# Performance work log

Hardware: AMD Instinct MI355X
Metric: run time of the kernel (lower is better)

Reference implementation:

```python
import jax, jax.numpy as jnp
import numpy as np

B, N, DIM, H, HD = 8, 1024, 512, 8, 64
INNER = H * HD  # 512
KS = 5


def setup_inputs() -> dict:
    key = jax.random.key(0)
    ks = jax.random.split(key, 9)
    r = lambda k, shape, s=1.0: jax.random.normal(k, shape, dtype=jnp.float32) * s
    return {
        "x_1": r(ks[0], (B, N, DIM)),
        "x_2": r(ks[1], (B, N, DIM)),
        "Wqkv1": r(ks[2], (DIM, 4 * INNER), 0.02),
        "Wqkv2": r(ks[3], (DIM, 4 * INNER), 0.02),
        "Wout1": r(ks[4], (INNER, DIM), 0.02),
        "bout1": jnp.zeros((DIM,), jnp.float32),
        "Wout2": r(ks[5], (INNER, DIM), 0.02),
        "bout2": jnp.zeros((DIM,), jnp.float32),
        "conv_w": r(ks[6], (N, 1, KS), 0.1),   # depthwise Conv1d weight [out=N, in/groups=1, k]
        "conv_b": r(ks[7], (N,), 0.02),
    }


def _split_heads(t):
    # 'b n (h d) -> b h n d'
    b, n, _ = t.shape
    return t.reshape(b, n, H, HD).transpose(0, 2, 1, 3)


def _merge_heads(t):
    # 'b h n d -> b n (h d)'
    b, h, n, d = t.shape
    return t.transpose(0, 2, 1, 3).reshape(b, n, h * d)


def reference(x_1, x_2, Wqkv1, Wqkv2, Wout1, bout1, Wout2, bout2, conv_w, conv_b):
    scale = HD ** (-0.5)
    q1, k1, v1, s1 = map(_split_heads, jnp.split(x_1 @ Wqkv1, 4, axis=-1))
    q2, k2, v2, s2 = map(_split_heads, jnp.split(x_2 @ Wqkv2, 4, axis=-1))

    dots1 = jnp.einsum('bhid,bhjd->bhij', q1, k1) * scale
    dots2 = jnp.einsum('bhid,bhjd->bhij', q2, k2) * scale

    MS = _merge_heads(s1 + s2)  # [b, n, inner_dim]
    # depthwise conv over the feature axis, channels = tokens (n), kernel 5 pad 2
    A = jax.lax.conv_general_dilated(
        MS, conv_w, window_strides=(1,), padding=((KS // 2, KS // 2),),
        dimension_numbers=('NCH', 'OIH', 'NCH'), feature_group_count=N,
    ) + conv_b[None, :, None]
    MSg = jax.nn.sigmoid(A) * MS
    MSh = _split_heads(MSg)
    dots3 = jnp.einsum('bhid,bhjd->bhij', MSh, MSh) * scale

    a1 = jax.nn.softmax(dots1, axis=-1)
    a2 = jax.nn.softmax(dots2, axis=-1)
    a3 = jax.nn.softmax(dots3, axis=-1)

    t1 = jnp.einsum('bhij,bhjd->bhid', a3, v1) + v1
    t1 = jnp.einsum('bhij,bhjd->bhid', a1, t1)
    t2 = jnp.einsum('bhij,bhjd->bhid', a3, v2) + v2
    t2 = jnp.einsum('bhij,bhjd->bhid', a2, t2)

    out1 = _merge_heads(t1) @ Wout1 + bout1
    out2 = _merge_heads(t2) @ Wout2 + bout2
    return (out1, out2)
```

## Files before the change

kernel.cpp:

```cpp
#include <hip/hip_runtime.h>
#include <hip/hip_bf16.h>

#define B_     8
#define N_     1024
#define DIM_   512
#define H_     8
#define HD_    64
#define INNER_ 512
#define QKVC   2048
#define M_     8192

typedef __attribute__((ext_vector_type(8))) short short8;
typedef __attribute__((ext_vector_type(4))) float f32x4;
#define MFMA_BF16 __builtin_amdgcn_mfma_f32_16x16x32_bf16

__device__ __forceinline__ unsigned short f2b(float x) {
    __hip_bfloat16 h = __float2bfloat16(x);
    unsigned short u; __builtin_memcpy(&u, &h, 2); return u;
}
__device__ __forceinline__ unsigned int packsplit(float x) {
    unsigned int hb = f2b(x);
    float fh = __uint_as_float(hb << 16);
    unsigned int lb = f2b(x - fh);
    return (hb << 16) | lb;
}
__device__ __forceinline__ void split8(const float* v, short8& h, short8& l) {
#pragma unroll
    for (int i = 0; i < 8; i++) {
        unsigned int hb = f2b(v[i]);
        float fh = __uint_as_float(hb << 16);
        h[i] = (short)hb; l[i] = (short)f2b(v[i] - fh);
    }
}
__device__ __forceinline__ void split2x2(float a, float b, unsigned int& h, unsigned int& l) {
    unsigned int ha = f2b(a), hb = f2b(b);
    float fa = __uint_as_float(ha << 16), fb = __uint_as_float(hb << 16);
    h = ha | (hb << 16);
    l = (unsigned int)f2b(a - fa) | ((unsigned int)f2b(b - fb) << 16);
}

__device__ __forceinline__ void gll16(const unsigned short* g, unsigned short* l) {
    __builtin_amdgcn_global_load_lds(
        (const __attribute__((address_space(1))) void*)g,
        (__attribute__((address_space(3))) void*)l, 16, 0, 0);
}

__global__ __launch_bounds__(256)
void pack_a_tiled(const float* __restrict__ in, unsigned short* __restrict__ out)
{
    size_t i = ((size_t)blockIdx.x * 256 + threadIdx.x) * 4;
    float4 v = *(const float4*)(in + i);
    const size_t R = i >> 9;
    const int k  = (int)(i & 511);
    const int kt = k >> 5, kk = k & 31;
    const int r  = (int)(R & 127);
    const size_t rt = R >> 7;
    unsigned short* tile = out + (((rt << 4) + kt) << 13) + r * 64;
    unsigned int h01, l01, h23, l23;
    split2x2(v.x, v.y, h01, l01);
    split2x2(v.z, v.w, h23, l23);
    uint2 hv; hv.x = h01; hv.y = h23;
    uint2 lv; lv.x = l01; lv.y = l23;
    const int s7 = r & 7;
    *(uint2*)&tile[(((kk >> 3)     ^ s7) << 3) + (kk & 7)] = hv;
    *(uint2*)&tile[((((kk >> 3)+4) ^ s7) << 3) + (kk & 7)] = lv;
}

__global__ __launch_bounds__(256)
void pack_w_tiled(const float* __restrict__ W, unsigned short* __restrict__ out, int N)
{
    const int n  = blockIdx.x * 256 + threadIdx.x;
    const int k0 = blockIdx.y * 4;
    float f0 = W[(size_t)(k0 + 0) * N + n];
    float f1 = W[(size_t)(k0 + 1) * N + n];
    float f2 = W[(size_t)(k0 + 2) * N + n];
    float f3 = W[(size_t)(k0 + 3) * N + n];
    const int r  = n & 127;
    const size_t rt = n >> 7;
    const int kt = k0 >> 5, kk = k0 & 31;
    unsigned short* tile = out + (((rt << 4) + kt) << 13) + r * 64;
    unsigned int h01, l01, h23, l23;
    split2x2(f0, f1, h01, l01);
    split2x2(f2, f3, h23, l23);
    uint2 hv; hv.x = h01; hv.y = h23;
    uint2 lv; lv.x = l01; lv.y = l23;
    const int s7 = r & 7;
    *(uint2*)&tile[(((kk >> 3)     ^ s7) << 3) + (kk & 7)] = hv;
    *(uint2*)&tile[((((kk >> 3)+4) ^ s7) << 3) + (kk & 7)] = lv;
}

__global__ __launch_bounds__(256)
void pack_wt(const float* __restrict__ W, unsigned int* __restrict__ Wt, int N)
{
    const int n = blockIdx.x * 256 + threadIdx.x;
    const int k0 = blockIdx.y * 4;
    uint4 p;
    p.x = packsplit(W[(size_t)(k0 + 0) * N + n]);
    p.y = packsplit(W[(size_t)(k0 + 1) * N + n]);
    p.z = packsplit(W[(size_t)(k0 + 2) * N + n]);
    p.w = packsplit(W[(size_t)(k0 + 3) * N + n]);
    *(uint4*)&Wt[(size_t)n * 512 + k0] = p;
}

template<bool BIAS, bool PACKK>
__global__ __launch_bounds__(256)
void gemm_gll(const unsigned short* __restrict__ At, const unsigned short* __restrict__ Bt,
              const float* __restrict__ bias, float* __restrict__ Cp,
              int M, int N)
{
    __shared__ __align__(16) unsigned short sA[128 * 64];
    __shared__ __align__(16) unsigned short sB[128 * 64];

    const int t    = threadIdx.x;
    const int lane = t & 63;
    const int w    = t >> 6;
    const int n16  = lane & 15, quad = lane >> 4;
    const int wm   = w >> 1, wn = w & 1;
    const int m0 = blockIdx.y * 128, n0 = blockIdx.x * 128;

    f32x4 acc[4][4];
#pragma unroll
    for (int mt = 0; mt < 4; mt++)
#pragma unroll
        for (int nt = 0; nt < 4; nt++) acc[mt][nt] = (f32x4){0.f, 0.f, 0.f, 0.f};

    const unsigned short* Ag = At + ((size_t)blockIdx.y << 4) * 8192 + (w * 64 + lane) * 8;
    const unsigned short* Bg = Bt + ((size_t)blockIdx.x << 4) * 8192 + (w * 64 + lane) * 8;
    unsigned short* sAw = &sA[w * 512];
    unsigned short* sBw = &sB[w * 512];

    for (int kt = 0; kt < 16; kt++) {
        __syncthreads();
        const size_t ko = (size_t)kt * 8192;
#pragma unroll
        for (int i = 0; i < 4; i++) {
            gll16(Ag + ko + i * 2048, sAw + i * 2048);
            gll16(Bg + ko + i * 2048, sBw + i * 2048);
        }
        __syncthreads();

        short8 Ah[4], Al[4];
#pragma unroll
        for (int mt = 0; mt < 4; mt++) {
            const int row = 64 * wm + 16 * mt + n16;
            const int base = row * 64;
            const int s7 = row & 7;
            Ah[mt] = *(const short8*)&sA[base + (((quad    ) ^ s7) << 3)];
            Al[mt] = *(const short8*)&sA[base + (((quad + 4) ^ s7) << 3)];
        }
#pragma unroll
        for (int nt = 0; nt < 4; nt++) {
            const int row = 64 * wn + 16 * nt + n16;
            const int base = row * 64;
            const int s7 = row & 7;
            short8 Bh = *(const short8*)&sB[base + (((quad    ) ^ s7) << 3)];
            short8 Bl = *(const short8*)&sB[base + (((quad + 4) ^ s7) << 3)];
#pragma unroll
            for (int mt = 0; mt < 4; mt++) {
                acc[mt][nt] = MFMA_BF16(Ah[mt], Bh, acc[mt][nt], 0, 0, 0);
                acc[mt][nt] = MFMA_BF16(Al[mt], Bh, acc[mt][nt], 0, 0, 0);
                acc[mt][nt] = MFMA_BF16(Ah[mt], Bl, acc[mt][nt], 0, 0, 0);
            }
        }
    }

    const bool packout = PACKK && ((n0 >> 9) == 1);
    float bv[4];
#pragma unroll
    for (int nt = 0; nt < 4; nt++)
        bv[nt] = BIAS ? bias[n0 + 64 * wn + 16 * nt + n16] : 0.f;
#pragma unroll
    for (int mt = 0; mt < 4; mt++) {
        const int rbase = m0 + 64 * wm + 16 * mt + 4 * quad;
#pragma unroll
        for (int r = 0; r < 4; r++) {
#pragma unroll
            for (int nt = 0; nt < 4; nt++) {
                const int col = n0 + 64 * wn + 16 * nt + n16;
                const size_t off = (size_t)(rbase + r) * N + col;
                const float v = acc[mt][nt][r] + bv[nt];
                if (packout) ((unsigned int*)Cp)[off] = packsplit(v);
                else         Cp[off] = v;
            }
        }
    }
}

template<bool BIAS, bool PACKK>
__global__ __launch_bounds__(256)
void gemm_mfma(const unsigned int* __restrict__ Ap, const unsigned int* __restrict__ Btp,
               const float* __restrict__ bias, float* __restrict__ Cp,
               int M, int N)
{
    const int K = 512;
    __shared__ __align__(16) unsigned short sA[128 * 64];
    __shared__ __align__(16) unsigned short sB[128 * 64];

    const int t    = threadIdx.x;
    const int lane = t & 63;
    const int w    = t >> 6;
    const int n16  = lane & 15, quad = lane >> 4;
    const int wm   = w >> 1, wn = w & 1;
    const int m0 = blockIdx.y * 128, n0 = blockIdx.x * 128;

    f32x4 acc[4][4];
#pragma unroll
    for (int mt = 0; mt < 4; mt++)
#pragma unroll
        for (int nt = 0; nt < 4; nt++) acc[mt][nt] = (f32x4){0.f, 0.f, 0.f, 0.f};

    const int srow = t >> 1;
    const int kb   = (t & 1) * 16;
    const unsigned int* ag = Ap  + (size_t)(m0 + srow) * K + kb;
    const unsigned int* bg = Btp + (size_t)(n0 + srow) * K + kb;
    const int s7s = srow & 7;
    unsigned short* swA = &sA[srow * 64];
    unsigned short* swB = &sB[srow * 64];

    for (int k0 = 0; k0 < K; k0 += 32) {
        __syncthreads();
#pragma unroll
        for (int i = 0; i < 4; i++) {
            const int kk = kb + i * 4;
            const int ch = kk >> 3;
            const int ho = kk & 4;
            const int c_hi = ((ch    ) ^ s7s) << 3;
            const int c_lo = ((ch + 4) ^ s7s) << 3;
            uint4 va = *(const uint4*)(ag + k0 + i * 4);
            uint4 vb = *(const uint4*)(bg + k0 + i * 4);
            uint2 ha, la, hb, lb;
            ha.x = (va.y & 0xFFFF0000u) | (va.x >> 16);
            ha.y = (va.w & 0xFFFF0000u) | (va.z >> 16);
            la.x = (va.y << 16) | (va.x & 0xFFFFu);
            la.y = (va.w << 16) | (va.z & 0xFFFFu);
            hb.x = (vb.y & 0xFFFF0000u) | (vb.x >> 16);
            hb.y = (vb.w & 0xFFFF0000u) | (vb.z >> 16);
            lb.x = (vb.y << 16) | (vb.x & 0xFFFFu);
            lb.y = (vb.w << 16) | (vb.z & 0xFFFFu);
            *(uint2*)&swA[c_hi + ho] = ha;
            *(uint2*)&swA[c_lo + ho] = la;
            *(uint2*)&swB[c_hi + ho] = hb;
            *(uint2*)&swB[c_lo + ho] = lb;
        }
        __syncthreads();

        short8 Ah[4], Al[4];
#pragma unroll
        for (int mt = 0; mt < 4; mt++) {
            const int row = 64 * wm + 16 * mt + n16;
            const int base = row * 64;
            const int s7 = row & 7;
            Ah[mt] = *(const short8*)&sA[base + (((quad    ) ^ s7) << 3)];
            Al[mt] = *(const short8*)&sA[base + (((quad + 4) ^ s7) << 3)];
        }
#pragma unroll
        for (int nt = 0; nt < 4; nt++) {
            const int row = 64 * wn + 16 * nt + n16;
            const int base = row * 64;
            const int s7 = row & 7;
            short8 Bh = *(const short8*)&sB[base + (((quad    ) ^ s7) << 3)];
            short8 Bl = *(const short8*)&sB[base + (((quad + 4) ^ s7) << 3)];
#pragma unroll
            for (int mt = 0; mt < 4; mt++) {
                acc[mt][nt] = MFMA_BF16(Ah[mt], Bh, acc[mt][nt], 0, 0, 0);
                acc[mt][nt] = MFMA_BF16(Al[mt], Bh, acc[mt][nt], 0, 0, 0);
                acc[mt][nt] = MFMA_BF16(Ah[mt], Bl, acc[mt][nt], 0, 0, 0);
            }
        }
    }

    const bool packout = PACKK && ((n0 >> 9) == 1);
    float bv[4];
#pragma unroll
    for (int nt = 0; nt < 4; nt++)
        bv[nt] = BIAS ? bias[n0 + 64 * wn + 16 * nt + n16] : 0.f;
#pragma unroll
    for (int mt = 0; mt < 4; mt++) {
        const int rbase = m0 + 64 * wm + 16 * mt + 4 * quad;
#pragma unroll
        for (int r = 0; r < 4; r++) {
#pragma unroll
            for (int nt = 0; nt < 4; nt++) {
                const int col = n0 + 64 * wn + 16 * nt + n16;
                const size_t off = (size_t)(rbase + r) * N + col;
                const float v = acc[mt][nt][r] + bv[nt];
                if (packout) ((unsigned int*)Cp)[off] = packsplit(v);
                else         Cp[off] = v;
            }
        }
    }
}

__global__ __launch_bounds__(128)
void convgate_kernel(const float* __restrict__ qkv1, const float* __restrict__ qkv2,
                     const float* __restrict__ convw,
                     const float* __restrict__ convb,
                     float* __restrict__ MSg, unsigned int* __restrict__ MSgp)
{
    __shared__ float ms[INNER_];
    const int blk = blockIdx.x;
    const int n = blk & (N_ - 1);
    const int t = threadIdx.x;

    const float4* q1 = (const float4*)(qkv1 + (size_t)blk * QKVC + 3 * INNER_);
    const float4* q2 = (const float4*)(qkv2 + (size_t)blk * QKVC + 3 * INNER_);
    float4 v1 = q1[t], v2 = q2[t];
    float4 s;
    s.x = v1.x + v2.x; s.y = v1.y + v2.y; s.z = v1.z + v2.z; s.w = v1.w + v2.w;
    *(float4*)&ms[t * 4] = s;
    __syncthreads();

    float w[5];
#pragma unroll
    for (int k = 0; k < 5; k++) w[k] = convw[n * 5 + k];
    const float cb = convb[n];

    float out[4];
#pragma unroll
    for (int ff = 0; ff < 4; ff++) {
        int f = t * 4 + ff;
        float A = cb;
#pragma unroll
        for (int k = 0; k < 5; k++) {
            int idx = f + k - 2;
            if (idx >= 0 && idx < INNER_) A += ms[idx] * w[k];
        }
        float sg = 1.f / (1.f + __expf(-A));
        out[ff] = ms[f] * sg;
    }
    *(float4*)&MSg[(size_t)blk * INNER_ + t * 4] = make_float4(out[0], out[1], out[2], out[3]);
    uint4 p;
    p.x = packsplit(out[0]); p.y = packsplit(out[1]);
    p.z = packsplit(out[2]); p.w = packsplit(out[3]);
    *(uint4*)&MSgp[(size_t)blk * INNER_ + t * 4] = p;
}

template<int NV, bool RESID, bool PACKO, int NPROB>
__global__ __launch_bounds__(512, 2)
void mattn_kernel(const float* __restrict__ Q0, const float* __restrict__ Q1,
                  const unsigned int* __restrict__ K0, const unsigned int* __restrict__ K1,
                  const float* __restrict__ VA0, const float* __restrict__ VA1,
                  const float* __restrict__ VB0, const float* __restrict__ VB1,
                  float* __restrict__ OA0, float* __restrict__ OA1,
                  float* __restrict__ OB0, float* __restrict__ OB1,
                  long long q_sb, long long q_sh, int q_sr,
                  long long k_sb, long long k_sh, int k_sr,
                  long long v_sb, long long v_sh, int v_sr,
                  long long o_sb, long long o_sh, int o_sr)
{
    __shared__ __align__(16) unsigned short sK[64 * 128];
    __shared__ __align__(16) unsigned short sV0[64 * 64];
    __shared__ __align__(16) unsigned short sV1[(NV == 2) ? 64 * 64 : 8];
    __shared__ __align__(16) unsigned short sP[128 * 64];

    const int t    = threadIdx.x;
    const int w    = t >> 6;
    const int lane = t & 63;
    const int n16  = lane & 15;
    const int quad = lane >> 4;

    const int bid = blockIdx.x;
    const int c   = bid & 7;
    const int r1  = bid >> 3;
    const int qt  = r1 & 7;
    const int r2  = r1 >> 3;
    const int g   = r2 & 7;
    const int p   = (NPROB == 2) ? (r2 >> 3) : 0;
    const int bh  = 8 * g + c;
    const int b = bh >> 3, h = bh & 7;
    const int i0 = qt * 128;

    const float* Qb        = (NPROB == 2 && p) ? Q1 : Q0;
    const unsigned int* Kb = (NPROB == 2 && p) ? K1 : K0;
    const float* VAb       = (NPROB == 2 && p) ? VA1 : VA0;
    float* OAb             = (NPROB == 2 && p) ? OA1 : OA0;

    const float* Qg        = Qb  + (size_t)b * q_sb + (size_t)h * q_sh;
    const unsigned int* Kg = Kb  + (size_t)b * k_sb + (size_t)h * k_sh;
    const float* V0g       = VAb + (size_t)b * v_sb + (size_t)h * v_sh;
    const float* V1g = (NV == 2) ? (VB0 + (size_t)b * v_sb + (size_t)h * v_sh) : nullptr;
    float* O0g = OAb + (size_t)b * o_sb + (size_t)h * o_sh;
    float* O1g = (NV == 2) ? (OB0 + (size_t)b * o_sb + (size_t)h * o_sh) : nullptr;

    short8 Qh[2], Ql[2];
#pragma unroll
    for (int s = 0; s < 2; s++) {
        const float* qp = Qg + (size_t)(i0 + 16 * w + n16) * q_sr + 32 * s + 8 * quad;
        float qv[8];
        float4 q0 = *(const float4*)qp;
        float4 q1 = *(const float4*)(qp + 4);
        qv[0]=q0.x; qv[1]=q0.y; qv[2]=q0.z; qv[3]=q0.w;
        qv[4]=q1.x; qv[5]=q1.y; qv[6]=q1.z; qv[7]=q1.w;
        split8(qv, Qh[s], Ql[s]);
    }

    float m_ = -1e30f, l_ = 0.f;
    f32x4 O0a[4], O1a[(NV == 2) ? 4 : 1];
#pragma unroll
    for (int nt = 0; nt < 4; nt++) O0a[nt] = (f32x4){0.f,0.f,0.f,0.f};
    if constexpr (NV == 2) {
#pragma unroll
        for (int nt = 0; nt < 4; nt++) O1a[nt] = (f32x4){0.f,0.f,0.f,0.f};
    }

    const float scale = 0.125f;
    const int prow = 16 * w + n16;
    const int krow = t >> 3, kfc = t & 7;
    const int vc = t & 15, vp = t >> 4;

    for (int j0 = 0; j0 < N_; j0 += 64) {
        __syncthreads();

        {
            const unsigned int* kp = Kg + (size_t)(j0 + krow) * k_sr + 8 * kfc;
            uint4 va = *(const uint4*)kp;
            uint4 vb = *(const uint4*)(kp + 4);
            uint4 hi, lo;
            hi.x = (va.x >> 16) | (va.y & 0xFFFF0000u);
            hi.y = (va.z >> 16) | (va.w & 0xFFFF0000u);
            hi.z = (vb.x >> 16) | (vb.y & 0xFFFF0000u);
            hi.w = (vb.z >> 16) | (vb.w & 0xFFFF0000u);
            lo.x = (va.x & 0xFFFFu) | (va.y << 16);
            lo.y = (va.z & 0xFFFFu) | (va.w << 16);
            lo.z = (vb.x & 0xFFFFu) | (vb.y << 16);
            lo.w = (vb.z & 0xFFFFu) | (vb.w << 16);
            const int r15 = krow & 15;
            *(uint4*)&sK[krow * 128 + (((kfc    ) ^ r15) << 3)] = hi;
            *(uint4*)&sK[krow * 128 + (((kfc + 8) ^ r15) << 3)] = lo;
        }
        {
            const int j = 2 * vp;
            const float* a0 = V0g + (size_t)(j0 + j) * v_sr + 4 * vc;
            float4 va = *(const float4*)a0;
            float4 vb = *(const float4*)(a0 + v_sr);
#pragma unroll
            for (int e = 0; e < 4; e++) {
                float fa = (e==0)?va.x:(e==1)?va.y:(e==2)?va.z:va.w;
                float fb = (e==0)?vb.x:(e==1)?vb.y:(e==2)?vb.z:vb.w;
                unsigned int u = (unsigned int)f2b(fa) | ((unsigned int)f2b(fb) << 16);
                const int d = 4 * vc + e;
                const int phys = (vp >> 2) ^ ((d ^ (d >> 2)) & 7);
                *(unsigned int*)&sV0[d * 64 + (phys << 3) + (j & 7)] = u;
            }
            if constexpr (NV == 2) {
                const float* a1 = V1g + (size_t)(j0 + j) * v_sr + 4 * vc;
                float4 wa = *(const float4*)a1;
                float4 wb = *(const float4*)(a1 + v_sr);
#pragma unroll
                for (int e = 0; e < 4; e++) {
                    float fa = (e==0)?wa.x:(e==1)?wa.y:(e==2)?wa.z:wa.w;
                    float fb = (e==0)?wb.x:(e==1)?wb.y:(e==2)?wb.z:wb.w;
                    unsigned int u = (unsigned int)f2b(fa) | ((unsigned int)f2b(fb) << 16);
                    const int d = 4 * vc + e;
                    const int phys = (vp >> 2) ^ ((d ^ (d >> 2)) & 7);
                    *(unsigned int*)&sV1[d * 64 + (phys << 3) + (j & 7)] = u;
                }
            }
        }
        __syncthreads();

        f32x4 accS[4];
#pragma unroll
        for (int mt = 0; mt < 4; mt++) accS[mt] = (f32x4){0.f,0.f,0.f,0.f};
#pragma unroll
        for (int s = 0; s < 2; s++) {
#pragma unroll
            for (int mt = 0; mt < 4; mt++) {
                const unsigned short* kb2 = &sK[(16 * mt + n16) * 128];
                short8 kh = *(const short8*)&kb2[(((4*s + quad)    ) ^ n16) << 3];
                short8 kl = *(const short8*)&kb2[(((4*s + quad) + 8) ^ n16) << 3];
                accS[mt] = MFMA_BF16(kl, Qh[s], accS[mt], 0, 0, 0);
                accS[mt] = MFMA_BF16(kh, Ql[s], accS[mt], 0, 0, 0);
                accS[mt] = MFMA_BF16(kh, Qh[s], accS[mt], 0, 0, 0);
            }
        }

        float tmax = -1e30f;
#pragma unroll
        for (int mt = 0; mt < 4; mt++)
#pragma unroll
            for (int r = 0; r < 4; r++) tmax = fmaxf(tmax, accS[mt][r]);
        tmax *= scale;
        tmax = fmaxf(tmax, __shfl_xor(tmax, 16));
        tmax = fmaxf(tmax, __shfl_xor(tmax, 32));
        const float mnew = fmaxf(m_, tmax);
        const float alpha = __expf(m_ - mnew);
        m_ = mnew;
        float rsum = 0.f;
#pragma unroll
        for (int mt = 0; mt < 4; mt++) {
            float p0 = __expf(accS[mt][0] * scale - mnew);
            float p1 = __expf(accS[mt][1] * scale - mnew);
            float p2 = __expf(accS[mt][2] * scale - mnew);
            float p3 = __expf(accS[mt][3] * scale - mnew);
            rsum += (p0 + p1) + (p2 + p3);
            uint2 u;
            u.x = (unsigned int)f2b(p0) | ((unsigned int)f2b(p1) << 16);
            u.y = (unsigned int)f2b(p2) | ((unsigned int)f2b(p3) << 16);
            const int phys = (2 * mt + (quad >> 1)) ^ (n16 & 7);
            *(uint2*)&sP[prow * 64 + (phys << 3) + 4 * (quad & 1)] = u;
        }
        rsum += __shfl_xor(rsum, 16);
        rsum += __shfl_xor(rsum, 32);
        l_ = l_ * alpha + rsum;

        float ar[4];
#pragma unroll
        for (int r = 0; r < 4; r++) ar[r] = __shfl(alpha, (quad << 2) + r);
#pragma unroll
        for (int nt = 0; nt < 4; nt++) {
#pragma unroll
            for (int r = 0; r < 4; r++) O0a[nt][r] *= ar[r];
            if constexpr (NV == 2)
#pragma unroll
                for (int r = 0; r < 4; r++) O1a[nt][r] *= ar[r];
        }

#pragma unroll
        for (int s = 0; s < 2; s++) {
            short8 Pf = *(const short8*)&sP[prow * 64 + (((4*s + quad) ^ (n16 & 7)) << 3)];
#pragma unroll
            for (int nt = 0; nt < 4; nt++) {
                const int d = 16 * nt + n16;
                const int phys = (4*s + quad) ^ ((d ^ (d >> 2)) & 7);
                short8 vf = *(const short8*)&sV0[d * 64 + (phys << 3)];
                O0a[nt] = MFMA_BF16(Pf, vf, O0a[nt], 0, 0, 0);
                if constexpr (NV == 2) {
                    short8 vf1 = *(const short8*)&sV1[d * 64 + (phys << 3)];
                    O1a[nt] = MFMA_BF16(Pf, vf1, O1a[nt], 0, 0, 0);
                }
            }
        }
    }

    float linv[4];
#pragma unroll
    for (int r = 0; r < 4; r++) linv[r] = 1.0f / __shfl(l_, (quad << 2) + r);
#pragma unroll
    for (int r = 0; r < 4; r++) {
        const int row = i0 + 16 * w + 4 * quad + r;
#pragma unroll
        for (int nt = 0; nt < 4; nt++) {
            const int col = 16 * nt + n16;
            float v = O0a[nt][r] * linv[r];
            if constexpr (RESID) v += V0g[(size_t)row * v_sr + col];
            if constexpr (PACKO)
                ((unsigned int*)O0g)[(size_t)row * o_sr + col] = packsplit(v);
            else
                O0g[(size_t)row * o_sr + col] = v;
            if constexpr (NV == 2) {
                float v1 = O1a[nt][r] * linv[r];
                if constexpr (RESID) v1 += V1g[(size_t)row * v_sr + col];
                if constexpr (PACKO)
                    ((unsigned int*)O1g)[(size_t)row * o_sr + col] = packsplit(v1);
                else
                    O1g[(size_t)row * o_sr + col] = v1;
            }
        }
    }
}

extern "C" void kernel_launch(void* const* d_in, const int* in_sizes, int n_in,
                              void* d_out, int out_size, void* d_ws, size_t ws_size,
                              hipStream_t stream)
{
    const float* x1    = (const float*)d_in[0];
    const float* x2    = (const float*)d_in[1];
    const float* Wqkv1 = (const float*)d_in[2];
    const float* Wqkv2 = (const float*)d_in[3];
    const float* Wout1 = (const float*)d_in[4];
    const float* bout1 = (const float*)d_in[5];
    const float* Wout2 = (const float*)d_in[6];
    const float* bout2 = (const float*)d_in[7];
    const float* convw = (const float*)d_in[8];
    const float* convb = (const float*)d_in[9];

    const size_t QKV_ELEMS = (size_t)M_ * QKVC;
    const size_t BND_ELEMS = (size_t)M_ * INNER_;
    if (ws_size < (2 * QKV_ELEMS + 5 * BND_ELEMS) * sizeof(float)) return;

    float* ws   = (float*)d_ws;
    float* qkv1 = ws;
    float* qkv2 = qkv1 + QKV_ELEMS;
    float* MSg  = qkv2 + QKV_ELEMS;
    float* u1   = MSg + BND_ELEMS;
    float* u2   = u1 + BND_ELEMS;
    float* t1m  = u2 + BND_ELEMS;
    float* t2m  = t1m + BND_ELEMS;

    unsigned short* x1t = (unsigned short*)t1m;
    unsigned short* x2t = (unsigned short*)t2m;
    unsigned int*   MSgp = (unsigned int*)t1m;
    unsigned short* w1t = (unsigned short*)u2;
    unsigned short* w2t = w1t + (size_t)QKVC * DIM_ * 2;
    unsigned int*   wo1pt = (unsigned int*)u1;
    unsigned int*   wo2pt = wo1pt + (size_t)DIM_ * DIM_;

    dim3 blk(256);

    pack_a_tiled<<<dim3(M_ * DIM_ / 1024), blk, 0, stream>>>(x1, x1t);
    pack_a_tiled<<<dim3(M_ * DIM_ / 1024), blk, 0, stream>>>(x2, x2t);
    pack_w_tiled<<<dim3(QKVC / 256, DIM_ / 4), blk, 0, stream>>>(Wqkv1, w1t, QKVC);
    pack_w_tiled<<<dim3(QKVC / 256, DIM_ / 4), blk, 0, stream>>>(Wqkv2, w2t, QKVC);

    gemm_gll<false, true><<<dim3(QKVC / 128, M_ / 128), blk, 0, stream>>>(
        x1t, w1t, nullptr, qkv1, M_, QKVC);
    gemm_gll<false, true><<<dim3(QKVC / 128, M_ / 128), blk, 0, stream>>>(
        x2t, w2t, nullptr, qkv2, M_, QKVC);

    convgate_kernel<<<dim3(M_), dim3(128), 0, stream>>>(qkv1, qkv2, convw, convb, MSg, MSgp);

    const long long msg_sb = (long long)N_ * INNER_, msg_sh = HD_;
    const int       msg_sr = INNER_;
    const long long qkv_sb = (long long)N_ * QKVC, qkv_sh = HD_;
    const int       qkv_sr = QKVC;
    const long long u_sb = (long long)H_ * N_ * HD_, u_sh = (long long)N_ * HD_;
    const int       u_sr = HD_;

    mattn_kernel<2, true, false, 1><<<dim3(512), dim3(512), 0, stream>>>(
        MSg, nullptr, MSgp, nullptr,
        qkv1 + 2 * INNER_, nullptr, qkv2 + 2 * INNER_, nullptr,
        u1, nullptr, u2, nullptr,
        msg_sb, msg_sh, msg_sr,
        msg_sb, msg_sh, msg_sr,
        qkv_sb, qkv_sh, qkv_sr,
        u_sb, u_sh, u_sr);

    mattn_kernel<1, false, true, 2><<<dim3(1024), dim3(512), 0, stream>>>(
        qkv1, qkv2,
        (const unsigned int*)qkv1 + INNER_, (const unsigned int*)qkv2 + INNER_,
        u1, u2, nullptr, nullptr,
        t1m, t2m, nullptr, nullptr,
        qkv_sb, qkv_sh, qkv_sr,
        qkv_sb, qkv_sh, qkv_sr,
        u_sb, u_sh, u_sr,
        msg_sb, msg_sh, msg_sr);

    pack_wt<<<dim3(DIM_ / 256, DIM_ / 4), blk, 0, stream>>>(Wout1, wo1pt, DIM_);
    pack_wt<<<dim3(DIM_ / 256, DIM_ / 4), blk, 0, stream>>>(Wout2, wo2pt, DIM_);

    float* out1 = (float*)d_out;
    float* out2 = out1 + (size_t)M_ * DIM_;
    gemm_mfma<true, false><<<dim3(DIM_ / 128, M_ / 128), blk, 0, stream>>>(
        (const unsigned int*)t1m, wo1pt, bout1, out1, M_, DIM_);
    gemm_mfma<true, false><<<dim3(DIM_ / 128, M_ / 128), blk, 0, stream>>>(
        (const unsigned int*)t2m, wo2pt, bout2, out2, M_, DIM_);
}
```

Baseline: 466.8 us.

## Pre-swizzle K into LDS image layout and use lazy exp2 softmax rescaling

```diff
diff --git a/kernel.cpp b/kernel.cpp
--- a/kernel.cpp
+++ b/kernel.cpp
@@ -44,6 +44,7 @@
         (const __attribute__((address_space(1))) void*)g,
         (__attribute__((address_space(3))) void*)l, 16, 0, 0);
 }
+
 
 __global__ __launch_bounds__(256)
 void pack_a_tiled(const float* __restrict__ in, unsigned short* __restrict__ out)
@@ -177,16 +178,26 @@
 #pragma unroll
             for (int nt = 0; nt < 4; nt++) {
                 const int col = n0 + 64 * wn + 16 * nt + n16;
-                const size_t off = (size_t)(rbase + r) * N + col;
+                const int row = rbase + r;
                 const float v = acc[mt][nt][r] + bv[nt];
-                if (packout) ((unsigned int*)Cp)[off] = packsplit(v);
-                else         Cp[off] = v;
-            }
-        }
-    }
-}
-
-template<bool BIAS, bool PACKK>
+                if (packout) {
+                    const int hh = (col >> 6) & 7, dd = col & 63, r15 = row & 15;
+                    unsigned int hb = f2b(v);
+                    float fh = __uint_as_float(hb << 16);
+                    unsigned short lb = f2b(v - fh);
+                    unsigned short* kim = (unsigned short*)Cp
+                        + (size_t)row * (2 * N) + 1024 + hh * 128 + (dd & 7);
+                    kim[(((dd >> 3)    ) ^ r15) << 3] = (unsigned short)hb;
+                    kim[(((dd >> 3) | 8) ^ r15) << 3] = lb;
+                } else {
+                    Cp[(size_t)row * N + col] = v;
+                }
+            }
+        }
+    }
+}
+
+template<bool BIAS>
 __global__ __launch_bounds__(256)
 void gemm_mfma(const unsigned int* __restrict__ Ap, const unsigned int* __restrict__ Btp,
                const float* __restrict__ bias, float* __restrict__ Cp,
@@ -269,7 +280,6 @@
         }
     }
 
-    const bool packout = PACKK && ((n0 >> 9) == 1);
     float bv[4];
 #pragma unroll
     for (int nt = 0; nt < 4; nt++)
@@ -282,10 +292,7 @@
 #pragma unroll
             for (int nt = 0; nt < 4; nt++) {
                 const int col = n0 + 64 * wn + 16 * nt + n16;
-                const size_t off = (size_t)(rbase + r) * N + col;
-                const float v = acc[mt][nt][r] + bv[nt];
-                if (packout) ((unsigned int*)Cp)[off] = packsplit(v);
-                else         Cp[off] = v;
+                Cp[(size_t)(rbase + r) * N + col] = acc[mt][nt][r] + bv[nt];
             }
         }
     }
@@ -295,11 +302,12 @@
 void convgate_kernel(const float* __restrict__ qkv1, const float* __restrict__ qkv2,
                      const float* __restrict__ convw,
                      const float* __restrict__ convb,
-                     float* __restrict__ MSg, unsigned int* __restrict__ MSgp)
+                     float* __restrict__ MSg, unsigned short* __restrict__ Kimg)
 {
     __shared__ float ms[INNER_];
     const int blk = blockIdx.x;
     const int n = blk & (N_ - 1);
+    const int b = blk >> 10;
     const int t = threadIdx.x;
 
     const float4* q1 = (const float4*)(qkv1 + (size_t)blk * QKVC + 3 * INNER_);
@@ -329,22 +337,37 @@
         out[ff] = ms[f] * sg;
     }
     *(float4*)&MSg[(size_t)blk * INNER_ + t * 4] = make_float4(out[0], out[1], out[2], out[3]);
-    uint4 p;
-    p.x = packsplit(out[0]); p.y = packsplit(out[1]);
-    p.z = packsplit(out[2]); p.w = packsplit(out[3]);
-    *(uint4*)&MSgp[(size_t)blk * INNER_ + t * 4] = p;
+
+    const int h  = t >> 4;
+    const int d0 = (4 * t) & 63;
+    const int r15 = n & 15;
+    unsigned short hs[4], ls[4];
+#pragma unroll
+    for (int e = 0; e < 4; e++) {
+        unsigned int hb = f2b(out[e]);
+        float fh = __uint_as_float(hb << 16);
+        hs[e] = (unsigned short)hb;
+        ls[e] = f2b(out[e] - fh);
+    }
+    unsigned short* kim = Kimg + ((size_t)(b * 8 + h) * 1024 + n) * 128 + (d0 & 7);
+    uint2 hv; hv.x = (unsigned int)hs[0] | ((unsigned int)hs[1] << 16);
+              hv.y = (unsigned int)hs[2] | ((unsigned int)hs[3] << 16);
+    uint2 lv; lv.x = (unsigned int)ls[0] | ((unsigned int)ls[1] << 16);
+              lv.y = (unsigned int)ls[2] | ((unsigned int)ls[3] << 16);
+    *(uint2*)&kim[(((d0 >> 3)    ) ^ r15) << 3] = hv;
+    *(uint2*)&kim[(((d0 >> 3) | 8) ^ r15) << 3] = lv;
 }
 
 template<int NV, bool RESID, bool PACKO, int NPROB>
 __global__ __launch_bounds__(512, 2)
 void mattn_kernel(const float* __restrict__ Q0, const float* __restrict__ Q1,
-                  const unsigned int* __restrict__ K0, const unsigned int* __restrict__ K1,
+                  const unsigned short* __restrict__ K0, const unsigned short* __restrict__ K1,
                   const float* __restrict__ VA0, const float* __restrict__ VA1,
                   const float* __restrict__ VB0, const float* __restrict__ VB1,
                   float* __restrict__ OA0, float* __restrict__ OA1,
                   float* __restrict__ OB0, float* __restrict__ OB1,
                   long long q_sb, long long q_sh, int q_sr,
-                  long long k_sb, long long k_sh, int k_sr,
+                  long long k_sb, long long k_sh, int k_rs,
                   long long v_sb, long long v_sh, int v_sr,
                   long long o_sb, long long o_sh, int o_sr)
 {
@@ -370,18 +393,19 @@
     const int b = bh >> 3, h = bh & 7;
     const int i0 = qt * 128;
 
-    const float* Qb        = (NPROB == 2 && p) ? Q1 : Q0;
-    const unsigned int* Kb = (NPROB == 2 && p) ? K1 : K0;
-    const float* VAb       = (NPROB == 2 && p) ? VA1 : VA0;
-    float* OAb             = (NPROB == 2 && p) ? OA1 : OA0;
-
-    const float* Qg        = Qb  + (size_t)b * q_sb + (size_t)h * q_sh;
-    const unsigned int* Kg = Kb  + (size_t)b * k_sb + (size_t)h * k_sh;
-    const float* V0g       = VAb + (size_t)b * v_sb + (size_t)h * v_sh;
+    const float* Qb          = (NPROB == 2 && p) ? Q1 : Q0;
+    const unsigned short* Kb = (NPROB == 2 && p) ? K1 : K0;
+    const float* VAb         = (NPROB == 2 && p) ? VA1 : VA0;
+    float* OAb               = (NPROB == 2 && p) ? OA1 : OA0;
+
+    const float* Qg          = Qb  + (size_t)b * q_sb + (size_t)h * q_sh;
+    const unsigned short* Kg = Kb  + (size_t)b * k_sb + (size_t)h * k_sh;
+    const float* V0g         = VAb + (size_t)b * v_sb + (size_t)h * v_sh;
     const float* V1g = (NV == 2) ? (VB0 + (size_t)b * v_sb + (size_t)h * v_sh) : nullptr;
     float* O0g = OAb + (size_t)b * o_sb + (size_t)h * o_sh;
     float* O1g = (NV == 2) ? (OB0 + (size_t)b * o_sb + (size_t)h * o_sh) : nullptr;
 
+    const float SC2 = 0.1803368801f;
     short8 Qh[2], Ql[2];
 #pragma unroll
     for (int s = 0; s < 2; s++) {
@@ -389,8 +413,8 @@
         float qv[8];
         float4 q0 = *(const float4*)qp;
         float4 q1 = *(const float4*)(qp + 4);
-        qv[0]=q0.x; qv[1]=q0.y; qv[2]=q0.z; qv[3]=q0.w;
-        qv[4]=q1.x; qv[5]=q1.y; qv[6]=q1.z; qv[7]=q1.w;
+        qv[0]=q0.x*SC2; qv[1]=q0.y*SC2; qv[2]=q0.z*SC2; qv[3]=q0.w*SC2;
+        qv[4]=q1.x*SC2; qv[5]=q1.y*SC2; qv[6]=q1.z*SC2; qv[7]=q1.w*SC2;
         split8(qv, Qh[s], Ql[s]);
     }
 
@@ -403,30 +427,20 @@
         for (int nt = 0; nt < 4; nt++) O1a[nt] = (f32x4){0.f,0.f,0.f,0.f};
     }
 
-    const float scale = 0.125f;
     const int prow = 16 * w + n16;
-    const int krow = t >> 3, kfc = t & 7;
     const int vc = t & 15, vp = t >> 4;
+
+    const unsigned short* kg_base = Kg + (size_t)((w << 2) + (lane >> 4)) * k_rs
+                                       + ((lane & 15) << 3);
+    unsigned short* sKw = &sK[w * 512];
 
     for (int j0 = 0; j0 < N_; j0 += 64) {
         __syncthreads();
 
         {
-            const unsigned int* kp = Kg + (size_t)(j0 + krow) * k_sr + 8 * kfc;
-            uint4 va = *(const uint4*)kp;
-            uint4 vb = *(const uint4*)(kp + 4);
-            uint4 hi, lo;
-            hi.x = (va.x >> 16) | (va.y & 0xFFFF0000u);
-            hi.y = (va.z >> 16) | (va.w & 0xFFFF0000u);
-            hi.z = (vb.x >> 16) | (vb.y & 0xFFFF0000u);
-            hi.w = (vb.z >> 16) | (vb.w & 0xFFFF0000u);
-            lo.x = (va.x & 0xFFFFu) | (va.y << 16);
-            lo.y = (va.z & 0xFFFFu) | (va.w << 16);
-            lo.z = (vb.x & 0xFFFFu) | (vb.y << 16);
-            lo.w = (vb.z & 0xFFFFu) | (vb.w << 16);
-            const int r15 = krow & 15;
-            *(uint4*)&sK[krow * 128 + (((kfc    ) ^ r15) << 3)] = hi;
-            *(uint4*)&sK[krow * 128 + (((kfc + 8) ^ r15) << 3)] = lo;
+            const unsigned short* kg = kg_base + (size_t)j0 * k_rs;
+            gll16(kg, sKw);
+            gll16(kg + (size_t)32 * k_rs, sKw + 4096);
         }
         {
             const int j = 2 * vp;
@@ -480,19 +494,32 @@
         for (int mt = 0; mt < 4; mt++)
 #pragma unroll
             for (int r = 0; r < 4; r++) tmax = fmaxf(tmax, accS[mt][r]);
-        tmax *= scale;
         tmax = fmaxf(tmax, __shfl_xor(tmax, 16));
         tmax = fmaxf(tmax, __shfl_xor(tmax, 32));
-        const float mnew = fmaxf(m_, tmax);
-        const float alpha = __expf(m_ - mnew);
-        m_ = mnew;
+        if (!__all(tmax <= m_ + 11.0f)) {
+            const float mnew = fmaxf(m_, tmax);
+            const float alpha = __builtin_amdgcn_exp2f(m_ - mnew);
+            m_ = mnew;
+            l_ *= alpha;
+            float ar[4];
+#pragma unroll
+            for (int r = 0; r < 4; r++) ar[r] = __shfl(alpha, (quad << 2) + r);
+#pragma unroll
+            for (int nt = 0; nt < 4; nt++) {
+#pragma unroll
+                for (int r = 0; r < 4; r++) O0a[nt][r] *= ar[r];
+                if constexpr (NV == 2)
+#pragma unroll
+                    for (int r = 0; r < 4; r++) O1a[nt][r] *= ar[r];
+            }
+        }
         float rsum = 0.f;
 #pragma unroll
         for (int mt = 0; mt < 4; mt++) {
-            float p0 = __expf(accS[mt][0] * scale - mnew);
-            float p1 = __expf(accS[mt][1] * scale - mnew);
-            float p2 = __expf(accS[mt][2] * scale - mnew);
-            float p3 = __expf(accS[mt][3] * scale - mnew);
+            float p0 = __builtin_amdgcn_exp2f(accS[mt][0] - m_);
+            float p1 = __builtin_amdgcn_exp2f(accS[mt][1] - m_);
+            float p2 = __builtin_amdgcn_exp2f(accS[mt][2] - m_);
+            float p3 = __builtin_amdgcn_exp2f(accS[mt][3] - m_);
             rsum += (p0 + p1) + (p2 + p3);
             uint2 u;
             u.x = (unsigned int)f2b(p0) | ((unsigned int)f2b(p1) << 16);
@@ -502,19 +529,7 @@
         }
         rsum += __shfl_xor(rsum, 16);
         rsum += __shfl_xor(rsum, 32);
-        l_ = l_ * alpha + rsum;
-
-        float ar[4];
-#pragma unroll
-        for (int r = 0; r < 4; r++) ar[r] = __shfl(alpha, (quad << 2) + r);
-#pragma unroll
-        for (int nt = 0; nt < 4; nt++) {
-#pragma unroll
-            for (int r = 0; r < 4; r++) O0a[nt][r] *= ar[r];
-            if constexpr (NV == 2)
-#pragma unroll
-                for (int r = 0; r < 4; r++) O1a[nt][r] *= ar[r];
-        }
+        l_ += rsum;
 
 #pragma unroll
         for (int s = 0; s < 2; s++) {
@@ -588,11 +603,11 @@
     float* t1m  = u2 + BND_ELEMS;
     float* t2m  = t1m + BND_ELEMS;
 
-    unsigned short* x1t = (unsigned short*)t1m;
-    unsigned short* x2t = (unsigned short*)t2m;
-    unsigned int*   MSgp = (unsigned int*)t1m;
-    unsigned short* w1t = (unsigned short*)u2;
-    unsigned short* w2t = w1t + (size_t)QKVC * DIM_ * 2;
+    unsigned short* x1t  = (unsigned short*)t1m;
+    unsigned short* x2t  = (unsigned short*)t2m;
+    unsigned short* KimgA = (unsigned short*)t1m;
+    unsigned short* w1t  = (unsigned short*)u2;
+    unsigned short* w2t  = w1t + (size_t)QKVC * DIM_ * 2;
     unsigned int*   wo1pt = (unsigned int*)u1;
     unsigned int*   wo2pt = wo1pt + (size_t)DIM_ * DIM_;
 
@@ -608,7 +623,8 @@
     gemm_gll<false, true><<<dim3(QKVC / 128, M_ / 128), blk, 0, stream>>>(
         x2t, w2t, nullptr, qkv2, M_, QKVC);
 
-    convgate_kernel<<<dim3(M_), dim3(128), 0, stream>>>(qkv1, qkv2, convw, convb, MSg, MSgp);
+    convgate_kernel<<<dim3(M_), dim3(128), 0, stream>>>(qkv1, qkv2, convw, convb,
+                                                        MSg, KimgA);
 
     const long long msg_sb = (long long)N_ * INNER_, msg_sh = HD_;
     const int       msg_sr = INNER_;
@@ -616,23 +632,27 @@
     const int       qkv_sr = QKVC;
     const long long u_sb = (long long)H_ * N_ * HD_, u_sh = (long long)N_ * HD_;
     const int       u_sr = HD_;
+    const long long kA_sb = (long long)8 * N_ * 128, kA_sh = (long long)N_ * 128;
+    const int       kA_rs = 128;
+    const long long kB_sb = (long long)N_ * QKVC * 2, kB_sh = 128;
+    const int       kB_rs = QKVC * 2;
 
     mattn_kernel<2, true, false, 1><<<dim3(512), dim3(512), 0, stream>>>(
-        MSg, nullptr, MSgp, nullptr,
+        MSg, nullptr, KimgA, nullptr,
         qkv1 + 2 * INNER_, nullptr, qkv2 + 2 * INNER_, nullptr,
         u1, nullptr, u2, nullptr,
         msg_sb, msg_sh, msg_sr,
-        msg_sb, msg_sh, msg_sr,
+        kA_sb, kA_sh, kA_rs,
         qkv_sb, qkv_sh, qkv_sr,
         u_sb, u_sh, u_sr);
 
     mattn_kernel<1, false, true, 2><<<dim3(1024), dim3(512), 0, stream>>>(
         qkv1, qkv2,
-        (const unsigned int*)qkv1 + INNER_, (const unsigned int*)qkv2 + INNER_,
+        (const unsigned short*)qkv1 + 1024, (const unsigned short*)qkv2 + 1024,
         u1, u2, nullptr, nullptr,
         t1m, t2m, nullptr, nullptr,
         qkv_sb, qkv_sh, qkv_sr,
-        qkv_sb, qkv_sh, qkv_sr,
+        kB_sb, kB_sh, kB_rs,
         u_sb, u_sh, u_sr,
         msg_sb, msg_sh, msg_sr);
 
@@ -641,8 +661,8 @@
 
     float* out1 = (float*)d_out;
     float* out2 = out1 + (size_t)M_ * DIM_;
-    gemm_mfma<true, false><<<dim3(DIM_ / 128, M_ / 128), blk, 0, stream>>>(
+    gemm_mfma<true><<<dim3(DIM_ / 128, M_ / 128), blk, 0, stream>>>(
         (const unsigned int*)t1m, wo1pt, bout1, out1, M_, DIM_);
-    gemm_mfma<true, false><<<dim3(DIM_ / 128, M_ / 128), blk, 0, stream>>>(
+    gemm_mfma<true><<<dim3(DIM_ / 128, M_ / 128), blk, 0, stream>>>(
         (const unsigned int*)t2m, wo2pt, bout2, out2, M_, DIM_);
 }
```

Result: no change. 466.0 us (-0.2%).
